# Optimization experiments

Measured on AMD Instinct MI355X. Metric: run time of the kernel, lower is better.

Reference implementation:

```python
import jax, jax.numpy as jnp
import numpy as np

CHUNK = 64
EPS = 1e-5


def segsum(a):
    # a: (..., T) -> (..., T, T) lower-triangular cumulative segment sums; -inf above diag
    T = a.shape[-1]
    cs = jnp.cumsum(a, axis=-1)
    ss = cs[..., :, None] - cs[..., None, :]
    mask = jnp.tril(jnp.ones((T, T), dtype=bool))
    return jnp.where(mask, ss, -jnp.inf)


def ssd(x, A, B, C, chunk):
    # x: (b, L, h, p), A: (b, L, h), B/C: (b, L, n)
    b, L, h, p = x.shape
    c = L // chunk
    x = x.reshape(b, c, chunk, h, p)
    A = A.reshape(b, c, chunk, h).transpose(0, 3, 1, 2)          # b h c l
    B = B.reshape(b, c, chunk, -1)                               # b c l n
    C = C.reshape(b, c, chunk, -1)                               # b c l n
    A_cum = jnp.cumsum(A, axis=-1)                               # b h c l
    Lmat = jnp.exp(segsum(A))                                    # b h c l l (causal decay)
    # intra-chunk (diagonal-block) output
    Y_diag = jnp.einsum('bcln,bcsn,bhcls,bcshp->bclhp', C, B, Lmat, x)
    # per-chunk states
    decay_states = jnp.exp(A_cum[..., -1:] - A_cum)              # b h c l
    states = jnp.einsum('bcln,bhcl,bclhp->bchpn', B, decay_states, x)
    states = jnp.concatenate([jnp.zeros_like(states[:, :1]), states], axis=1)  # b (c+1) h p n
    # inter-chunk recurrence via chunk-level segsum
    A_last = jnp.pad(A_cum[..., -1], ((0, 0), (0, 0), (1, 0)))   # b h (c+1)
    decay_chunk = jnp.exp(segsum(A_last))                        # b h (c+1) (c+1)
    new_states = jnp.einsum('bhzc,bchpn->bzhpn', decay_chunk, states)
    states, final = new_states[:, :-1], new_states[:, -1:]
    Y_off = jnp.einsum('bcln,bchpn,bhcl->bclhp', C, states, jnp.exp(A_cum))
    return (Y_diag + Y_off).reshape(b, L, h, p), final


def mamba2(x, W_in, conv_w, conv_b, dt_bias, A_log, D, norm_w, W_out):
    d_inner = norm_w.shape[0]
    nheads = dt_bias.shape[0]
    d_state = (conv_b.shape[0] - d_inner) // 2
    headdim = d_inner // nheads
    k_conv = conv_w.shape[0]
    b, L, _ = x.shape

    zxbcdt = x @ W_in                                            # (b, L, 2*d_inner+2*n+h)
    z = zxbcdt[..., :d_inner]
    xBC = zxbcdt[..., d_inner:2 * d_inner + 2 * d_state]
    dt = jax.nn.softplus(zxbcdt[..., 2 * d_inner + 2 * d_state:] + dt_bias)  # (b, L, h)
    A = -jnp.exp(A_log)                                          # (h,)

    # causal depthwise conv (zero init conv state == left-pad k_conv-1 zeros) + silu
    xp = jnp.pad(xBC, ((0, 0), (k_conv - 1, 0), (0, 0)))
    xBC = jax.lax.conv_general_dilated(
        xp, conv_w, (1,), 'VALID',
        dimension_numbers=('NWC', 'WIO', 'NWC'),
        feature_group_count=conv_b.shape[0])
    xBC = jax.nn.silu(xBC + conv_b)

    xs = xBC[..., :d_inner].reshape(b, L, nheads, headdim)       # (b, L, h, p)
    Bm = xBC[..., d_inner:d_inner + d_state]                     # (b, L, n)
    Cm = xBC[..., d_inner + d_state:]                            # (b, L, n)

    Y, _ = ssd(xs * dt[..., None], A * dt, Bm, Cm, CHUNK)
    Y = Y + xs * D                                               # D: (h, 1) broadcasts over p
    y = Y.reshape(b, L, d_inner)

    # gated RMSNorm
    y = y * jax.nn.silu(z)
    y = y * jax.lax.rsqrt(jnp.mean(y * y, axis=-1, keepdims=True) + EPS) * norm_w
    return y @ W_out


def setup_inputs():
    key = jax.random.key(0)
    ks = jax.random.split(key, 8)
    B, L, d_model = 2, 4096, 1024
    expand, d_state, k_conv, headdim = 2, 128, 4, 64
    d_inner = expand * d_model
    nheads = d_inner // headdim
    d_in_proj = 2 * d_inner + 2 * d_state + nheads
    conv_dim = d_inner + 2 * d_state
    return {
        'x': jax.random.normal(ks[0], (B, L, d_model), jnp.float32),
        'W_in': jax.random.normal(ks[1], (d_model, d_in_proj), jnp.float32) / np.sqrt(d_model).astype(np.float32),
        'conv_w': jax.random.normal(ks[2], (k_conv, 1, conv_dim), jnp.float32) / np.sqrt(k_conv).astype(np.float32),
        'conv_b': jnp.zeros((conv_dim,), jnp.float32),
        'dt_bias': jax.random.normal(ks[3], (nheads,), jnp.float32) * 0.5 - 2.0,
        'A_log': jnp.log(1.0 + 15.0 * jax.random.uniform(ks[4], (nheads,), jnp.float32)),
        'D': jax.random.normal(ks[5], (nheads, 1), jnp.float32),
        'norm_w': jnp.ones((d_inner,), jnp.float32),
        'W_out': jax.random.normal(ks[6], (d_inner, d_model), jnp.float32) / np.sqrt(d_inner).astype(np.float32),
    }


def reference(x, W_in, conv_w, conv_b, dt_bias, A_log, D, norm_w, W_out):
    return mamba2(x, W_in, conv_w, conv_b, dt_bias, A_log, D, norm_w, W_out)
```

## Files before the change

### kernel.cpp

```cpp
#include <hip/hip_runtime.h>
#include <hip/hip_fp16.h>

typedef _Float16 f16;
typedef _Float16 f16x4 __attribute__((ext_vector_type(4)));
typedef _Float16 f16x8 __attribute__((ext_vector_type(8)));
typedef float f32x4 __attribute__((ext_vector_type(4)));

#define DEV __device__ __forceinline__

constexpr int BB    = 2;
constexpr int LL    = 4096;
constexpr int DM    = 1024;
constexpr int DIN   = 2048;
constexpr int DST   = 128;
constexpr int NH    = 32;
constexpr int HD    = 64;
constexpr int NC    = 64;
constexpr int MROWS = BB * LL;
constexpr int NPROJ = 2*DIN + 2*DST + NH;
constexpr int NZ    = 2*DIN + 2*DST;
constexpr int CONVD = DIN + 2*DST;
constexpr int DT_OFF = 2*DIN + 2*DST;
constexpr int BOFF  = DIN;
constexpr int COFF  = DIN + DST;

DEV float silu_f(float v) { return v / (1.f + __expf(-v)); }

DEV void gload_lds16(const f16* gsrc, f16* lds_dst) {
  __builtin_amdgcn_global_load_lds(
      (const __attribute__((address_space(1))) void*)gsrc,
      (__attribute__((address_space(3))) void*)lds_dst, 16, 0, 0);
}

__global__ __launch_bounds__(256)
void tof16_kernel(const float* __restrict__ src, f16* __restrict__ dst, int n8) {
  int i = blockIdx.x * 256 + threadIdx.x;
  if (i >= n8) return;
  f32x4 a = *(const f32x4*)(src + (size_t)i*8);
  f32x4 b = *(const f32x4*)(src + (size_t)i*8 + 4);
  f16x8 o;
#pragma unroll
  for (int j = 0; j < 4; ++j) { o[j] = (f16)a[j]; o[4+j] = (f16)b[j]; }
  *(f16x8*)(dst + (size_t)i*8) = o;
}

__global__ __launch_bounds__(256)
void transpose_f32_to_f16(const float* __restrict__ src, f16* __restrict__ dst,
                          int K, int N, int srcLd) {
  __shared__ float tbuf[32][33];
  int n0 = blockIdx.x * 32, k0 = blockIdx.y * 32;
  int tx = threadIdx.x & 31, ty = threadIdx.x >> 5;
  for (int i = ty; i < 32; i += 8)
    tbuf[i][tx] = src[(size_t)(k0 + i)*srcLd + n0 + tx];
  __syncthreads();
  for (int i = ty; i < 32; i += 8)
    dst[(size_t)(n0 + i)*K + (k0 + tx)] = (f16)tbuf[tx][i];
}

template<int BM, int BN, int WM_, int WN_, bool C16>
__global__ __launch_bounds__(WM_*WN_*64, 2)
void gemm_t(const f16* __restrict__ A, const f16* __restrict__ Bt,
            void* __restrict__ Cp, int M, int N, int K, int ldc) {
  constexpr int THREADS = WM_*WN_*64;
  constexpr int WTM = BM/WM_, WTN = BN/WN_;
  constexpr int FM = WTM/16, FN = WTN/16;
  constexpr int LA = BM*4/THREADS, LB = BN*4/THREADS;
  constexpr int L = LA + LB;
  __shared__ f16 As[3][BM*32];
  __shared__ f16 Bs[3][BN*32];
  const int nbn = N / BN;
  const int bm = blockIdx.x / nbn, bn = blockIdx.x % nbn;
  const int tid = threadIdx.x;
  const int wave = tid >> 6, lane = tid & 63;
  const int lrow = lane & 15, kgrp = lane >> 4;
  const int wm = wave / WN_, wn = wave % WN_;
  const int nt = K >> 5;
  const int bcol8 = (kgrp ^ ((lrow ^ (lrow >> 2)) & 3)) * 8;

  const f16* aptr[LA];
  const f16* bptr[LB];
#pragma unroll
  for (int i = 0; i < LA; ++i) {
    int s = tid + i*THREADS, row = s >> 2;
    int g = (s & 3) ^ ((row ^ (row >> 2)) & 3);
    aptr[i] = A + (size_t)(bm*BM + row)*K + g*8;
  }
#pragma unroll
  for (int i = 0; i < LB; ++i) {
    int s = tid + i*THREADS, row = s >> 2;
    int g = (s & 3) ^ ((row ^ (row >> 2)) & 3);
    bptr[i] = Bt + (size_t)(bn*BN + row)*K + g*8;
  }

  f32x4 acc[FM][FN] = {};

  auto STAGE = [&](int buf, int t) {
#pragma unroll
    for (int i = 0; i < LA; ++i)
      gload_lds16(aptr[i] + (size_t)t*32, As[buf] + (wave*64 + i*THREADS)*8);
#pragma unroll
    for (int i = 0; i < LB; ++i)
      gload_lds16(bptr[i] + (size_t)t*32, Bs[buf] + (wave*64 + i*THREADS)*8);
  };
  auto WAITL = [&]() {
    if constexpr (L == 2)      asm volatile("s_waitcnt vmcnt(2)" ::: "memory");
    else if constexpr (L == 3) asm volatile("s_waitcnt vmcnt(3)" ::: "memory");
    else if constexpr (L == 4) asm volatile("s_waitcnt vmcnt(4)" ::: "memory");
    else if constexpr (L == 6) asm volatile("s_waitcnt vmcnt(6)" ::: "memory");
    else                       asm volatile("s_waitcnt vmcnt(0)" ::: "memory");
  };

  STAGE(0, 0);
  if (nt > 1) {
    STAGE(1, 1);
    WAITL();
  } else {
    asm volatile("s_waitcnt vmcnt(0)" ::: "memory");
  }
  __builtin_amdgcn_s_barrier();
  __builtin_amdgcn_sched_barrier(0);

  for (int t = 0; t < nt; ++t) {
    const int cur = t % 3;
    if (t + 2 < nt) STAGE((t + 2) % 3, t + 2);
    const f16* Ab = As[cur];
    const f16* Bb = Bs[cur];
    f16x8 bf[FN];
#pragma unroll
    for (int n = 0; n < FN; ++n)
      bf[n] = *(const f16x8*)(Bb + (wn*WTN + n*16 + lrow)*32 + bcol8);
#pragma unroll
    for (int m = 0; m < FM; ++m) {
      f16x8 af = *(const f16x8*)(Ab + (wm*WTM + m*16 + lrow)*32 + bcol8);
#pragma unroll
      for (int n = 0; n < FN; ++n)
        acc[m][n] = __builtin_amdgcn_mfma_f32_16x16x32_f16(af, bf[n], acc[m][n], 0, 0, 0);
    }
    if (t + 1 < nt) {
      if (t + 2 < nt) WAITL();
      else            asm volatile("s_waitcnt vmcnt(0)" ::: "memory");
      __builtin_amdgcn_s_barrier();
      __builtin_amdgcn_sched_barrier(0);
    }
  }

  int crow0 = bm*BM + wm*WTM, ccol0 = bn*BN + wn*WTN;
#pragma unroll
  for (int m = 0; m < FM; ++m)
#pragma unroll
    for (int n = 0; n < FN; ++n) {
      int r0 = crow0 + m*16 + (lane >> 4)*4;
      int c0 = ccol0 + n*16 + (lane & 15);
#pragma unroll
      for (int r = 0; r < 4; ++r) {
        if constexpr (C16) {
          f16* C = (f16*)Cp;
          C[(size_t)(r0 + r)*ldc + c0] = (f16)acc[m][n][r];
        } else {
          float* C = (float*)Cp;
          C[(size_t)(r0 + r)*ldc + c0] = acc[m][n][r];
        }
      }
    }
}

__global__ __launch_bounds__(256)
void dt_kernel(const float* __restrict__ x, const float* __restrict__ Win,
               const float* __restrict__ dt_bias, float* __restrict__ dt) {
  __shared__ float xs[64][132];
  __shared__ float ws[128][32];
  int r0 = blockIdx.x * 64;
  int t = threadIdx.x;
  int r = t >> 2, c0 = (t & 3) * 8;
  float acc[8] = {};
  for (int kt = 0; kt < 1024; kt += 128) {
    __syncthreads();
#pragma unroll
    for (int i = 0; i < 8; ++i) {
      int idx4 = t + i*256;
      int rr = idx4 >> 5, c4 = (idx4 & 31) * 4;
      *(f32x4*)&xs[rr][c4] = *(const f32x4*)(x + (size_t)(r0 + rr)*1024 + kt + c4);
    }
#pragma unroll
    for (int i = 0; i < 4; ++i) {
      int idx4 = t + i*256;
      int rr = idx4 >> 3, c4 = (idx4 & 7) * 4;
      *(f32x4*)&ws[rr][c4] = *(const f32x4*)(Win + (size_t)(kt + rr)*NPROJ + DT_OFF + c4);
    }
    __syncthreads();
#pragma unroll 8
    for (int k = 0; k < 128; ++k) {
      float xv = xs[r][k];
      f32x4 w0 = *(const f32x4*)&ws[k][c0];
      f32x4 w1 = *(const f32x4*)&ws[k][c0 + 4];
#pragma unroll
      for (int j = 0; j < 4; ++j) { acc[j] += xv * w0[j]; acc[4+j] += xv * w1[j]; }
    }
  }
#pragma unroll
  for (int j = 0; j < 8; ++j) {
    float v = acc[j] + dt_bias[c0 + j];
    float sp = (v > 20.f) ? v : log1pf(__expf(v));
    dt[(size_t)(r0 + r)*NH + c0 + j] = sp;
  }
}

__global__ __launch_bounds__(256)
void conv_kernel(const f16* __restrict__ zxh, const float* __restrict__ cw,
                 const float* __restrict__ cb, f16* __restrict__ out) {
  int i = blockIdx.x * 256 + threadIdx.x;
  int row = i / (CONVD/8);
  int c8  = (i - row*(CONVD/8)) * 8;
  int lb = row & (LL - 1);
  f32x4 a0 = *(const f32x4*)(cb + c8);
  f32x4 a1 = *(const f32x4*)(cb + c8 + 4);
#pragma unroll
  for (int j = 0; j < 4; ++j) {
    int lsrc = lb - 3 + j;
    if (lsrc >= 0) {
      f16x8 v = *(const f16x8*)(zxh + (size_t)(row - 3 + j)*NZ + BOFF + c8);
      f32x4 w0 = *(const f32x4*)(cw + j*CONVD + c8);
      f32x4 w1 = *(const f32x4*)(cw + j*CONVD + c8 + 4);
#pragma unroll
      for (int jj = 0; jj < 4; ++jj) {
        a0[jj] += (float)v[jj]   * w0[jj];
        a1[jj] += (float)v[4+jj] * w1[jj];
      }
    }
  }
  f16x8 o;
#pragma unroll
  for (int jj = 0; jj < 4; ++jj) {
    o[jj]   = (f16)silu_f(a0[jj]);
    o[4+jj] = (f16)silu_f(a1[jj]);
  }
  *(f16x8*)(out + (size_t)row*CONVD + c8) = o;
}

__global__ __launch_bounds__(256)
void acum_kernel(const float* __restrict__ dt, const float* __restrict__ A_log,
                 float* __restrict__ Acum) {
  int bc = blockIdx.x;
  int wave = threadIdx.x >> 6, lane = threadIdx.x & 63;
  int row = bc*64 + lane;
  for (int hh = 0; hh < 8; ++hh) {
    int h = wave*8 + hh;
    float A = -__expf(A_log[h]);
    float v = A * dt[(size_t)row*NH + h];
#pragma unroll
    for (int off = 1; off < 64; off <<= 1) {
      float u = __shfl_up(v, off);
      if (lane >= off) v += u;
    }
    Acum[((size_t)bc*NH + h)*64 + lane] = v;
  }
}

__global__ __launch_bounds__(256)
void gbuf_kernel(const f16* __restrict__ xbc, f16* __restrict__ G) {
  __shared__ float Cs[64][128];
  __shared__ float Bsm[64][128];
  int bc = blockIdx.x;
  int row0 = bc * 64;
  int t = threadIdx.x;
#pragma unroll
  for (int i = 0; i < 4; ++i) {
    int idx = t + i*256;
    int r = idx >> 4, c8 = (idx & 15) * 8;
    f16x8 cv = *(const f16x8*)(xbc + (size_t)(row0 + r)*CONVD + COFF + c8);
    f16x8 bv = *(const f16x8*)(xbc + (size_t)(row0 + r)*CONVD + BOFF + c8);
    f32x4 c0v = {(float)cv[0], (float)cv[1], (float)cv[2], (float)cv[3]};
    f32x4 c1v = {(float)cv[4], (float)cv[5], (float)cv[6], (float)cv[7]};
    f32x4 b0v = {(float)bv[0], (float)bv[1], (float)bv[2], (float)bv[3]};
    f32x4 b1v = {(float)bv[4], (float)bv[5], (float)bv[6], (float)bv[7]};
    *(f32x4*)&Cs[r][c8]      = c0v;  *(f32x4*)&Cs[r][c8 + 4]  = c1v;
    *(f32x4*)&Bsm[r][c8]     = b0v;  *(f32x4*)&Bsm[r][c8 + 4] = b1v;
  }
  __syncthreads();
  int l0 = (t >> 4)*4, s0 = (t & 15)*4;
  float acc[4][4] = {};
  for (int n4 = 0; n4 < 128; n4 += 4) {
    f32x4 cv[4], bv[4];
#pragma unroll
    for (int i = 0; i < 4; ++i) cv[i] = *(const f32x4*)&Cs[l0 + i][n4];
#pragma unroll
    for (int j = 0; j < 4; ++j) bv[j] = *(const f32x4*)&Bsm[s0 + j][n4];
#pragma unroll
    for (int i = 0; i < 4; ++i)
#pragma unroll
      for (int j = 0; j < 4; ++j)
        acc[i][j] += cv[i][0]*bv[j][0] + cv[i][1]*bv[j][1] + cv[i][2]*bv[j][2] + cv[i][3]*bv[j][3];
  }
#pragma unroll
  for (int i = 0; i < 4; ++i) {
    f16x4 v = {(f16)acc[i][0], (f16)acc[i][1], (f16)acc[i][2], (f16)acc[i][3]};
    *(f16x4*)(G + ((size_t)bc*64 + l0 + i)*64 + s0) = v;
  }
}

__global__ __launch_bounds__(256)
void ssd_a_kernel(const f16* __restrict__ xbc, const float* __restrict__ dtb,
                  const f16* __restrict__ Gg, const float* __restrict__ Acum,
                  f16* __restrict__ Ybuf, f16* __restrict__ states) {
  __shared__ union {
    struct { f16 XdT[64][72]; f16 Gt[64][72]; f16 BT[128][72]; } s;
    float Yl[64][68];
    float Sl[64][132];
  } u;
  __shared__ float ac[64], dts[64];
  int bc = blockIdx.x >> 5, h = blockIdx.x & 31;
  int row0 = bc*64, t = threadIdx.x;
  if (t < 64) {
    ac[t]  = Acum[((size_t)bc*NH + h)*64 + t];
    dts[t] = dtb[(size_t)(row0 + t)*NH + h];
  }
  __syncthreads();
  float ac63 = ac[63];
#pragma unroll
  for (int i = 0; i < 2; ++i) {
    int idx = t + i*256; int l = idx >> 3, p8 = (idx & 7)*8;
    f16x8 v = *(const f16x8*)(xbc + (size_t)(row0 + l)*CONVD + h*HD + p8);
    float d = dts[l];
#pragma unroll
    for (int j = 0; j < 8; ++j) u.s.XdT[p8 + j][l] = (f16)((float)v[j]*d);
  }
#pragma unroll
  for (int i = 0; i < 4; ++i) {
    int idx = t + i*256; int l = idx >> 4, n8 = (idx & 15)*8;
    f16x8 v = *(const f16x8*)(xbc + (size_t)(row0 + l)*CONVD + BOFF + n8);
    float dl = __expf(ac63 - ac[l]);
#pragma unroll
    for (int j = 0; j < 8; ++j) u.s.BT[n8 + j][l] = (f16)((float)v[j]*dl);
  }
#pragma unroll
  for (int i = 0; i < 2; ++i) {
    int idx = t + i*256; int l = idx >> 3, s8 = (idx & 7)*8;
    f16x8 g = *(const f16x8*)(Gg + (size_t)bc*4096 + l*64 + s8);
    float al = ac[l];
    f16x8 o;
#pragma unroll
    for (int j = 0; j < 8; ++j) {
      int s = s8 + j;
      o[j] = (l >= s) ? (f16)((float)g[j] * __expf(al - ac[s])) : (f16)0.f;
    }
    *(f16x8*)&u.s.Gt[l][s8] = o;
  }
  __syncthreads();
  int wave = t >> 6, lane = t & 63;
  int lrow = lane & 15, kgrp = lane >> 4;
  f32x4 yacc[4] = {};
  f32x4 sacc[8] = {};
#pragma unroll
  for (int kk = 0; kk < 64; kk += 32) {
    f16x8 afy = *(const f16x8*)&u.s.Gt[wave*16 + lrow][kk + kgrp*8];
    f16x8 afs = *(const f16x8*)&u.s.XdT[wave*16 + lrow][kk + kgrp*8];
#pragma unroll
    for (int n = 0; n < 4; ++n) {
      f16x8 bf = *(const f16x8*)&u.s.XdT[n*16 + lrow][kk + kgrp*8];
      yacc[n] = __builtin_amdgcn_mfma_f32_16x16x32_f16(afy, bf, yacc[n], 0, 0, 0);
    }
#pragma unroll
    for (int n = 0; n < 8; ++n) {
      f16x8 bf = *(const f16x8*)&u.s.BT[n*16 + lrow][kk + kgrp*8];
      sacc[n] = __builtin_amdgcn_mfma_f32_16x16x32_f16(afs, bf, sacc[n], 0, 0, 0);
    }
  }
  __syncthreads();
#pragma unroll
  for (int n = 0; n < 4; ++n)
#pragma unroll
    for (int r = 0; r < 4; ++r)
      u.Yl[wave*16 + kgrp*4 + r][n*16 + lrow] = yacc[n][r];
  __syncthreads();
#pragma unroll
  for (int i = 0; i < 2; ++i) {
    int idx = t + i*256; int l = idx >> 3, p8 = (idx & 7)*8;
    f16x8 o;
#pragma unroll
    for (int j = 0; j < 8; ++j) o[j] = (f16)u.Yl[l][p8 + j];
    *(f16x8*)(Ybuf + (size_t)(row0 + l)*DIN + h*HD + p8) = o;
  }
  __syncthreads();
#pragma unroll
  for (int n = 0; n < 8; ++n)
#pragma unroll
    for (int r = 0; r < 4; ++r)
      u.Sl[wave*16 + kgrp*4 + r][n*16 + lrow] = sacc[n][r];
  __syncthreads();
  size_t sb = ((size_t)bc*NH + h)*8192;
#pragma unroll
  for (int i = 0; i < 4; ++i) {
    int idx = t + i*256; int p = idx >> 4, n8 = (idx & 15)*8;
    f16x8 o;
#pragma unroll
    for (int j = 0; j < 8; ++j) o[j] = (f16)u.Sl[p][n8 + j];
    *(f16x8*)(states + sb + (size_t)p*128 + n8) = o;
  }
}

__global__ __launch_bounds__(256)
void scan_kernel(f16* __restrict__ states, const float* __restrict__ Acum) {
  int bid = blockIdx.x;
  int bh = bid >> 3, pgrp = bid & 7;
  int b = bh >> 5, h = bh & 31;
  int t = threadIdx.x;
  int p = pgrp*8 + (t >> 5), n4 = (t & 31) * 4;
  size_t off = (size_t)p*128 + n4;
  f32x4 carry = {0.f, 0.f, 0.f, 0.f};
  for (int c = 0; c < NC; ++c) {
    size_t base = ((size_t)(b*NC + c)*NH + h)*8192;
    f16x4 cv = *(f16x4*)(states + base + off);
    f16x4 st;
#pragma unroll
    for (int j = 0; j < 4; ++j) st[j] = (f16)carry[j];
    *(f16x4*)(states + base + off) = st;
    float tc = __expf(Acum[((size_t)(b*NC + c)*NH + h)*64 + 63]);
#pragma unroll
    for (int j = 0; j < 4; ++j) carry[j] = carry[j]*tc + (float)cv[j];
  }
}

__global__ __launch_bounds__(256)
void yoff_kernel(const f16* __restrict__ xbc, const f16* __restrict__ zxh,
                 const f16* __restrict__ states, const float* __restrict__ Acum,
                 const float* __restrict__ Dp, f16* __restrict__ Ybuf) {
  __shared__ union {
    struct { f16 Ch[64][136]; f16 Sin[64][136]; } s;
    float Yl[64][68];
  } u;
  __shared__ float eac[64];
  int bc = blockIdx.x >> 5, h = blockIdx.x & 31;
  int row0 = bc*64, t = threadIdx.x;
  if (t < 64) eac[t] = __expf(Acum[((size_t)bc*NH + h)*64 + t]);
  size_t sb = ((size_t)bc*NH + h)*8192;
#pragma unroll
  for (int i = 0; i < 4; ++i) {
    int idx = t + i*256; int r = idx >> 4, c8 = (idx & 15)*8;
    *(f16x8*)&u.s.Ch[r][c8]  = *(const f16x8*)(xbc + (size_t)(row0 + r)*CONVD + COFF + c8);
    *(f16x8*)&u.s.Sin[r][c8] = *(const f16x8*)(states + sb + (size_t)r*128 + c8);
  }
  __syncthreads();
  int wave = t >> 6, lane = t & 63;
  int lrow = lane & 15, kgrp = lane >> 4;
  f32x4 acc[4] = {};
#pragma unroll
  for (int kk = 0; kk < 128; kk += 32) {
    f16x8 af = *(const f16x8*)&u.s.Ch[wave*16 + lrow][kk + kgrp*8];
#pragma unroll
    for (int n = 0; n < 4; ++n) {
      f16x8 bf = *(const f16x8*)&u.s.Sin[n*16 + lrow][kk + kgrp*8];
      acc[n] = __builtin_amdgcn_mfma_f32_16x16x32_f16(af, bf, acc[n], 0, 0, 0);
    }
  }
  __syncthreads();
#pragma unroll
  for (int n = 0; n < 4; ++n)
#pragma unroll
    for (int r = 0; r < 4; ++r)
      u.Yl[wave*16 + kgrp*4 + r][n*16 + lrow] = acc[n][r];
  __syncthreads();
  float Dh = Dp[h];
#pragma unroll
  for (int i = 0; i < 2; ++i) {
    int idx = t + i*256; int l = idx >> 3, p8 = (idx & 7)*8;
    int row = row0 + l;
    f16x8 yd = *(const f16x8*)(Ybuf + (size_t)row*DIN + h*HD + p8);
    f16x8 zh = *(const f16x8*)(zxh + (size_t)row*NZ + h*HD + p8);
    f16x8 xs = *(const f16x8*)(xbc + (size_t)row*CONVD + h*HD + p8);
    float e = eac[l];
    f16x8 o;
#pragma unroll
    for (int j = 0; j < 8; ++j) {
      float yv = (float)yd[j] + e*u.Yl[l][p8 + j] + (float)xs[j]*Dh;
      o[j] = (f16)(yv * silu_f((float)zh[j]));
    }
    *(f16x8*)(Ybuf + (size_t)row*DIN + h*HD + p8) = o;
  }
}

__global__ __launch_bounds__(256)
void rms_kernel(const f16* __restrict__ yg, const float* __restrict__ nw,
                f16* __restrict__ yh) {
  __shared__ float red[4];
  int row = blockIdx.x, t = threadIdx.x;
  f16x8 v = *(const f16x8*)(yg + (size_t)row*DIN + t*8);
  float f[8];
  float ss = 0.f;
#pragma unroll
  for (int j = 0; j < 8; ++j) { f[j] = (float)v[j]; ss += f[j]*f[j]; }
#pragma unroll
  for (int off = 32; off > 0; off >>= 1) ss += __shfl_down(ss, off);
  if ((t & 63) == 0) red[t >> 6] = ss;
  __syncthreads();
  float tot = red[0] + red[1] + red[2] + red[3];
  float sc = rsqrtf(tot * (1.f/2048.f) + 1e-5f);
  f32x4 w0 = *(const f32x4*)(nw + t*8);
  f32x4 w1 = *(const f32x4*)(nw + t*8 + 4);
  f16x8 o;
#pragma unroll
  for (int j = 0; j < 4; ++j) {
    o[j]   = (f16)(f[j]   * sc * w0[j]);
    o[4+j] = (f16)(f[4+j] * sc * w1[j]);
  }
  *(f16x8*)(yh + (size_t)row*DIN + t*8) = o;
}

extern "C" void kernel_launch(void* const* d_in, const int* in_sizes, int n_in,
                              void* d_out, int out_size, void* d_ws, size_t ws_size,
                              hipStream_t stream) {
  const float* x       = (const float*)d_in[0];
  const float* W_in    = (const float*)d_in[1];
  const float* conv_w  = (const float*)d_in[2];
  const float* conv_b  = (const float*)d_in[3];
  const float* dt_bias = (const float*)d_in[4];
  const float* A_log   = (const float*)d_in[5];
  const float* Dp      = (const float*)d_in[6];
  const float* norm_w  = (const float*)d_in[7];
  const float* W_out   = (const float*)d_in[8];

  constexpr size_t WS_NEED = 213909504;
  if (ws_size < WS_NEED) return;

  char* w = (char*)d_ws;
  f16*   states = (f16*)(w + 0);
  f16*   winT   = (f16*)(w + 0);
  f16*   yh     = (f16*)(w + 0);
  f16*   xh     = (f16*)(w + 33554432);
  f16*   woutT  = (f16*)(w + 33554432);
  f16*   zxh    = (f16*)(w + 67108864);
  f16*   xbcc   = (f16*)(w + 138412032);
  f16*   Ybuf   = (f16*)(w + 176160768);
  float* dtb    = (float*)(w + 209715200);
  float* Acum   = (float*)(w + 210763776);
  f16*   Gg     = (f16*)(w + 211812352);

  tof16_kernel<<<4096, 256, 0, stream>>>(x, xh, MROWS*DM/8);
  transpose_f32_to_f16<<<dim3(NZ/32, DM/32), 256, 0, stream>>>(W_in, winT, DM, NZ, NPROJ);
  gemm_t<256,128,4,2,true><<<(MROWS/256)*(NZ/128), 512, 0, stream>>>(xh, winT, zxh, MROWS, NZ, DM, NZ);
  dt_kernel<<<MROWS/64, 256, 0, stream>>>(x, W_in, dt_bias, dtb);
  conv_kernel<<<MROWS*(CONVD/8)/256, 256, 0, stream>>>(zxh, conv_w, conv_b, xbcc);
  acum_kernel<<<BB*NC, 256, 0, stream>>>(dtb, A_log, Acum);
  gbuf_kernel<<<BB*NC, 256, 0, stream>>>(xbcc, Gg);
  ssd_a_kernel<<<BB*NC*NH, 256, 0, stream>>>(xbcc, dtb, Gg, Acum, Ybuf, states);
  scan_kernel<<<BB*NH*8, 256, 0, stream>>>(states, Acum);
  yoff_kernel<<<BB*NC*NH, 256, 0, stream>>>(xbcc, zxh, states, Acum, Dp, Ybuf);
  transpose_f32_to_f16<<<dim3(DM/32, DIN/32), 256, 0, stream>>>(W_out, woutT, DIN, DM, DM);
  rms_kernel<<<MROWS, 256, 0, stream>>>(Ybuf, norm_w, yh);
  gemm_t<128,128,2,2,false><<<(MROWS/128)*(DM/128), 256, 0, stream>>>(yh, woutT, d_out, MROWS, DM, DIN, DM);
}
```

Before: 429.9 us.

## Fuse acum into dt kernel and move intra-chunk Y_diag into yoff kernel

The chunk-cumulative A scan now runs at the end of dt_kernel from shared-memory dt values, which removes the separate acum_kernel launch. The intra-chunk diagonal output (G masked by decay times X·dt) moves from the states kernel into yoff_kernel and stays in LDS, so the fp16 Ybuf round trip through global memory is gone. In exchange yoff_kernel does more work and uses more shared memory, which may lower occupancy, and the states kernel becomes lighter.

```diff
diff --git a/kernel.cpp b/kernel.cpp
--- a/kernel.cpp
+++ b/kernel.cpp
@@ -111,12 +111,8 @@
   };
 
   STAGE(0, 0);
-  if (nt > 1) {
-    STAGE(1, 1);
-    WAITL();
-  } else {
-    asm volatile("s_waitcnt vmcnt(0)" ::: "memory");
-  }
+  if (nt > 1) { STAGE(1, 1); WAITL(); }
+  else        { asm volatile("s_waitcnt vmcnt(0)" ::: "memory"); }
   __builtin_amdgcn_s_barrier();
   __builtin_amdgcn_sched_barrier(0);
 
@@ -166,10 +162,13 @@
 
 __global__ __launch_bounds__(256)
 void dt_kernel(const float* __restrict__ x, const float* __restrict__ Win,
-               const float* __restrict__ dt_bias, float* __restrict__ dt) {
+               const float* __restrict__ dt_bias, const float* __restrict__ A_log,
+               float* __restrict__ dt, float* __restrict__ Acum) {
   __shared__ float xs[64][132];
   __shared__ float ws[128][32];
-  int r0 = blockIdx.x * 64;
+  __shared__ float dts[64][32];
+  int bc = blockIdx.x;
+  int r0 = bc * 64;
   int t = threadIdx.x;
   int r = t >> 2, c0 = (t & 3) * 8;
   float acc[8] = {};
@@ -202,6 +201,20 @@
     float v = acc[j] + dt_bias[c0 + j];
     float sp = (v > 20.f) ? v : log1pf(__expf(v));
     dt[(size_t)(r0 + r)*NH + c0 + j] = sp;
+    dts[r][c0 + j] = sp;
+  }
+  __syncthreads();
+  int wave = t >> 6, lane = t & 63;
+  for (int hh = 0; hh < 8; ++hh) {
+    int h = wave*8 + hh;
+    float A = -__expf(A_log[h]);
+    float v = A * dts[lane][h];
+#pragma unroll
+    for (int off = 1; off < 64; off <<= 1) {
+      float u = __shfl_up(v, off);
+      if (lane >= off) v += u;
+    }
+    Acum[((size_t)bc*NH + h)*64 + lane] = v;
   }
 }
 
@@ -235,25 +248,6 @@
     o[4+jj] = (f16)silu_f(a1[jj]);
   }
   *(f16x8*)(out + (size_t)row*CONVD + c8) = o;
-}
-
-__global__ __launch_bounds__(256)
-void acum_kernel(const float* __restrict__ dt, const float* __restrict__ A_log,
-                 float* __restrict__ Acum) {
-  int bc = blockIdx.x;
-  int wave = threadIdx.x >> 6, lane = threadIdx.x & 63;
-  int row = bc*64 + lane;
-  for (int hh = 0; hh < 8; ++hh) {
-    int h = wave*8 + hh;
-    float A = -__expf(A_log[h]);
-    float v = A * dt[(size_t)row*NH + h];
-#pragma unroll
-    for (int off = 1; off < 64; off <<= 1) {
-      float u = __shfl_up(v, off);
-      if (lane >= off) v += u;
-    }
-    Acum[((size_t)bc*NH + h)*64 + lane] = v;
-  }
 }
 
 __global__ __launch_bounds__(256)
@@ -299,12 +293,10 @@
 }
 
 __global__ __launch_bounds__(256)
-void ssd_a_kernel(const f16* __restrict__ xbc, const float* __restrict__ dtb,
-                  const f16* __restrict__ Gg, const float* __restrict__ Acum,
-                  f16* __restrict__ Ybuf, f16* __restrict__ states) {
+void ssd_states_kernel(const f16* __restrict__ xbc, const float* __restrict__ dtb,
+                       const float* __restrict__ Acum, f16* __restrict__ states) {
   __shared__ union {
-    struct { f16 XdT[64][72]; f16 Gt[64][72]; f16 BT[128][72]; } s;
-    float Yl[64][68];
+    struct { f16 XdT[64][72]; f16 BT[128][72]; } s;
     float Sl[64][132];
   } u;
   __shared__ float ac[64], dts[64];
@@ -332,53 +324,18 @@
 #pragma unroll
     for (int j = 0; j < 8; ++j) u.s.BT[n8 + j][l] = (f16)((float)v[j]*dl);
   }
-#pragma unroll
-  for (int i = 0; i < 2; ++i) {
-    int idx = t + i*256; int l = idx >> 3, s8 = (idx & 7)*8;
-    f16x8 g = *(const f16x8*)(Gg + (size_t)bc*4096 + l*64 + s8);
-    float al = ac[l];
-    f16x8 o;
-#pragma unroll
-    for (int j = 0; j < 8; ++j) {
-      int s = s8 + j;
-      o[j] = (l >= s) ? (f16)((float)g[j] * __expf(al - ac[s])) : (f16)0.f;
-    }
-    *(f16x8*)&u.s.Gt[l][s8] = o;
-  }
   __syncthreads();
   int wave = t >> 6, lane = t & 63;
   int lrow = lane & 15, kgrp = lane >> 4;
-  f32x4 yacc[4] = {};
   f32x4 sacc[8] = {};
 #pragma unroll
   for (int kk = 0; kk < 64; kk += 32) {
-    f16x8 afy = *(const f16x8*)&u.s.Gt[wave*16 + lrow][kk + kgrp*8];
     f16x8 afs = *(const f16x8*)&u.s.XdT[wave*16 + lrow][kk + kgrp*8];
-#pragma unroll
-    for (int n = 0; n < 4; ++n) {
-      f16x8 bf = *(const f16x8*)&u.s.XdT[n*16 + lrow][kk + kgrp*8];
-      yacc[n] = __builtin_amdgcn_mfma_f32_16x16x32_f16(afy, bf, yacc[n], 0, 0, 0);
-    }
 #pragma unroll
     for (int n = 0; n < 8; ++n) {
       f16x8 bf = *(const f16x8*)&u.s.BT[n*16 + lrow][kk + kgrp*8];
       sacc[n] = __builtin_amdgcn_mfma_f32_16x16x32_f16(afs, bf, sacc[n], 0, 0, 0);
     }
-  }
-  __syncthreads();
-#pragma unroll
-  for (int n = 0; n < 4; ++n)
-#pragma unroll
-    for (int r = 0; r < 4; ++r)
-      u.Yl[wave*16 + kgrp*4 + r][n*16 + lrow] = yacc[n][r];
-  __syncthreads();
-#pragma unroll
-  for (int i = 0; i < 2; ++i) {
-    int idx = t + i*256; int l = idx >> 3, p8 = (idx & 7)*8;
-    f16x8 o;
-#pragma unroll
-    for (int j = 0; j < 8; ++j) o[j] = (f16)u.Yl[l][p8 + j];
-    *(f16x8*)(Ybuf + (size_t)(row0 + l)*DIN + h*HD + p8) = o;
   }
   __syncthreads();
 #pragma unroll
@@ -422,33 +379,80 @@
 
 __global__ __launch_bounds__(256)
 void yoff_kernel(const f16* __restrict__ xbc, const f16* __restrict__ zxh,
-                 const f16* __restrict__ states, const float* __restrict__ Acum,
+                 const f16* __restrict__ Gg, const f16* __restrict__ states,
+                 const float* __restrict__ dtb, const float* __restrict__ Acum,
                  const float* __restrict__ Dp, f16* __restrict__ Ybuf) {
   __shared__ union {
-    struct { f16 Ch[64][136]; f16 Sin[64][136]; } s;
-    float Yl[64][68];
+    struct { f16 Gt[64][72]; f16 XdT[64][72]; } a;
+    struct { f16 Ch[64][136]; f16 Sin[64][136]; } b;
+    float Yl2[64][68];
   } u;
-  __shared__ float eac[64];
+  __shared__ float Yl[64][68];
+  __shared__ float ac[64], dts[64], eac[64];
   int bc = blockIdx.x >> 5, h = blockIdx.x & 31;
   int row0 = bc*64, t = threadIdx.x;
-  if (t < 64) eac[t] = __expf(Acum[((size_t)bc*NH + h)*64 + t]);
+  if (t < 64) {
+    float a0 = Acum[((size_t)bc*NH + h)*64 + t];
+    ac[t]  = a0;
+    eac[t] = __expf(a0);
+    dts[t] = dtb[(size_t)(row0 + t)*NH + h];
+  }
+  __syncthreads();
+#pragma unroll
+  for (int i = 0; i < 2; ++i) {
+    int idx = t + i*256; int l = idx >> 3, p8 = (idx & 7)*8;
+    f16x8 v = *(const f16x8*)(xbc + (size_t)(row0 + l)*CONVD + h*HD + p8);
+    float d = dts[l];
+#pragma unroll
+    for (int j = 0; j < 8; ++j) u.a.XdT[p8 + j][l] = (f16)((float)v[j]*d);
+  }
+#pragma unroll
+  for (int i = 0; i < 2; ++i) {
+    int idx = t + i*256; int l = idx >> 3, s8 = (idx & 7)*8;
+    f16x8 g = *(const f16x8*)(Gg + (size_t)bc*4096 + l*64 + s8);
+    float al = ac[l];
+    f16x8 o;
+#pragma unroll
+    for (int j = 0; j < 8; ++j) {
+      int s = s8 + j;
+      o[j] = (l >= s) ? (f16)((float)g[j] * __expf(al - ac[s])) : (f16)0.f;
+    }
+    *(f16x8*)&u.a.Gt[l][s8] = o;
+  }
+  __syncthreads();
+  int wave = t >> 6, lane = t & 63;
+  int lrow = lane & 15, kgrp = lane >> 4;
+  f32x4 yacc[4] = {};
+#pragma unroll
+  for (int kk = 0; kk < 64; kk += 32) {
+    f16x8 afy = *(const f16x8*)&u.a.Gt[wave*16 + lrow][kk + kgrp*8];
+#pragma unroll
+    for (int n = 0; n < 4; ++n) {
+      f16x8 bf = *(const f16x8*)&u.a.XdT[n*16 + lrow][kk + kgrp*8];
+      yacc[n] = __builtin_amdgcn_mfma_f32_16x16x32_f16(afy, bf, yacc[n], 0, 0, 0);
+    }
+  }
+  __syncthreads();
+#pragma unroll
+  for (int n = 0; n < 4; ++n)
+#pragma unroll
+    for (int r = 0; r < 4; ++r)
+      Yl[wave*16 + kgrp*4 + r][n*16 + lrow] = yacc[n][r];
   size_t sb = ((size_t)bc*NH + h)*8192;
 #pragma unroll
   for (int i = 0; i < 4; ++i) {
     int idx = t + i*256; int r = idx >> 4, c8 = (idx & 15)*8;
-    *(f16x8*)&u.s.Ch[r][c8]  = *(const f16x8*)(xbc + (size_t)(row0 + r)*CONVD + COFF + c8);
-    *(f16x8*)&u.s.Sin[r][c8] = *(const f16x8*)(states + sb + (size_t)r*128 + c8);
-  }
-  __syncthreads();
-  int wave = t >> 6, lane = t & 63;
-  int lrow = lane & 15, kgrp = lane >> 4;
+    *(f16x8*)&u.b.Ch[r][c8]  = *(const f16x8*)(xbc + (size_t)(row0 + r)*CONVD + COFF + c8);
+    *(f16x8*)&u.b.Sin[r][c8] = *(const f16x8*)(states + sb + (size_t)r*128 + c8);
+  }
+  __syncthreads();
   f32x4 acc[4] = {};
 #pragma unroll
   for (int kk = 0; kk < 128; kk += 32) {
-    f16x8 af = *(const f16x8*)&u.s.Ch[wave*16 + lrow][kk + kgrp*8];
+    f16x8 af = *(const f16x8*)&u.b.Ch[wave*16 + lrow][kk + kgrp*8];
 #pragma unroll
     for (int n = 0; n < 4; ++n) {
-      f16x8 bf = *(const f16x8*)&u.s.Sin[n*16 + lrow][kk + kgrp*8];
+      f16x8 bf = *(const f16x8*)&u.b.Sin[n*16 + lrow][kk + kgrp*8];
       acc[n] = __builtin_amdgcn_mfma_f32_16x16x32_f16(af, bf, acc[n], 0, 0, 0);
     }
   }
@@ -457,21 +461,20 @@
   for (int n = 0; n < 4; ++n)
 #pragma unroll
     for (int r = 0; r < 4; ++r)
-      u.Yl[wave*16 + kgrp*4 + r][n*16 + lrow] = acc[n][r];
+      u.Yl2[wave*16 + kgrp*4 + r][n*16 + lrow] = acc[n][r];
   __syncthreads();
   float Dh = Dp[h];
 #pragma unroll
   for (int i = 0; i < 2; ++i) {
     int idx = t + i*256; int l = idx >> 3, p8 = (idx & 7)*8;
     int row = row0 + l;
-    f16x8 yd = *(const f16x8*)(Ybuf + (size_t)row*DIN + h*HD + p8);
     f16x8 zh = *(const f16x8*)(zxh + (size_t)row*NZ + h*HD + p8);
     f16x8 xs = *(const f16x8*)(xbc + (size_t)row*CONVD + h*HD + p8);
     float e = eac[l];
     f16x8 o;
 #pragma unroll
     for (int j = 0; j < 8; ++j) {
-      float yv = (float)yd[j] + e*u.Yl[l][p8 + j] + (float)xs[j]*Dh;
+      float yv = Yl[l][p8 + j] + e*u.Yl2[l][p8 + j] + (float)xs[j]*Dh;
       o[j] = (f16)(yv * silu_f((float)zh[j]));
     }
     *(f16x8*)(Ybuf + (size_t)row*DIN + h*HD + p8) = o;
@@ -537,13 +540,12 @@
   tof16_kernel<<<4096, 256, 0, stream>>>(x, xh, MROWS*DM/8);
   transpose_f32_to_f16<<<dim3(NZ/32, DM/32), 256, 0, stream>>>(W_in, winT, DM, NZ, NPROJ);
   gemm_t<256,128,4,2,true><<<(MROWS/256)*(NZ/128), 512, 0, stream>>>(xh, winT, zxh, MROWS, NZ, DM, NZ);
-  dt_kernel<<<MROWS/64, 256, 0, stream>>>(x, W_in, dt_bias, dtb);
+  dt_kernel<<<MROWS/64, 256, 0, stream>>>(x, W_in, dt_bias, A_log, dtb, Acum);
   conv_kernel<<<MROWS*(CONVD/8)/256, 256, 0, stream>>>(zxh, conv_w, conv_b, xbcc);
-  acum_kernel<<<BB*NC, 256, 0, stream>>>(dtb, A_log, Acum);
   gbuf_kernel<<<BB*NC, 256, 0, stream>>>(xbcc, Gg);
-  ssd_a_kernel<<<BB*NC*NH, 256, 0, stream>>>(xbcc, dtb, Gg, Acum, Ybuf, states);
+  ssd_states_kernel<<<BB*NC*NH, 256, 0, stream>>>(xbcc, dtb, Acum, states);
   scan_kernel<<<BB*NH*8, 256, 0, stream>>>(states, Acum);
-  yoff_kernel<<<BB*NC*NH, 256, 0, stream>>>(xbcc, zxh, states, Acum, Dp, Ybuf);
+  yoff_kernel<<<BB*NC*NH, 256, 0, stream>>>(xbcc, zxh, Gg, states, dtb, Acum, Dp, Ybuf);
   transpose_f32_to_f16<<<dim3(DM/32, DIN/32), 256, 0, stream>>>(W_out, woutT, DIN, DM, DM);
   rms_kernel<<<MROWS, 256, 0, stream>>>(Ybuf, norm_w, yh);
   gemm_t<128,128,2,2,false><<<(MROWS/128)*(DM/128), 256, 0, stream>>>(yh, woutT, d_out, MROWS, DM, DIN, DM);
```

Measured after the change: 434.9 us. No clear change (+1.2%).
